# Performance work log

Measured on AMD Instinct MI355X. Metric: run time of the kernel, lower is better.

## Reference

```python
import jax, jax.numpy as jnp
import numpy as np

RADIUS = 9.0
GROUPS = 4
BLK = 64  # row block for streaming the N x N pairwise convolution


def leaky(x):
    return jnp.where(x >= 0, x, 0.2 * x)


def group_norm(x, gamma, beta, eps=1e-5):
    # x: (N, C); matches torch.nn.GroupNorm(GROUPS, C) applied to (1, C, N)
    N, C = x.shape
    xg = x.T.reshape(GROUPS, (C // GROUPS) * N)
    m = xg.mean(axis=1, keepdims=True)
    v = ((xg - m) ** 2).mean(axis=1, keepdims=True)
    xg = (xg - m) / jnp.sqrt(v + eps)
    return xg.reshape(C, N).T * gamma + beta


def tangent_vectors(n):
    # Duff et al. orthonormal tangent basis; n: (N,3) unit normals -> (N,2,3)
    x, y, z = n[:, 0], n[:, 1], n[:, 2]
    s = jnp.where(z >= 0, 1.0, -1.0)
    a = -1.0 / (s + z)
    b = x * y * a
    uv = jnp.stack([1 + s * x * x * a, s * b, -s * x, b, s + y * y * a, -y], axis=-1)
    return uv.reshape(-1, 2, 3)


def load_mesh(xyz, normals, weights):
    # Build oriented local frames nuv (N,3,3) as in dMaSIFConv_seg.load_mesh
    p = xyz / RADIUS
    uv = tangent_vectors(normals)                  # (N,2,3)
    diff = p[None, :, :] - p[:, None, :]           # (N,N,3): x_j - x_i
    d2 = jnp.sum(diff * diff, axis=-1)             # (N,N)
    cos = normals @ normals.T                      # (N,N)
    window = jnp.exp(-d2 * (2.0 - cos) ** 2)       # pseudo-geodesic Gaussian
    X = jnp.einsum('ikd,ijd->ijk', uv, diff)       # (N,N,2) tangent coords
    ov = jnp.einsum('ij,j,ijk->ik', window, weights[:, 0], X) + 1e-5  # (N,2)
    nrm = jnp.maximum(jnp.linalg.norm(ov, axis=-1, keepdims=True), 1e-12)
    ov = ov / nrm                                  # F.normalize
    ex, ey = ov[:, :1], ov[:, 1:]
    u, v = uv[:, 0, :], uv[:, 1, :]
    return jnp.stack([normals, ex * u + ey * v, -ey * u + ex * v], axis=1)


def dmasif_conv(points, nuv, feats,
                ni_w1, ni_b1, ni_w2, ni_b2, gn_in_g, gn_in_b,
                cv_a1, cv_b1, cv_a2, cv_b2,
                no_w1, no_b1, no_w2, no_b2, gn_out_g, gn_out_b):
    N = points.shape[0]
    H = ni_w1.shape[0]
    O = no_w1.shape[0]
    # net_in + GroupNorm
    h = leaky(feats @ ni_w1.T + ni_b1)
    h = leaky(h @ ni_w2.T + ni_b2)
    h = group_norm(h, gn_in_g, gn_in_b)            # (N,H)
    p = points / (np.sqrt(2.0) * RADIUS)
    n = jax.lax.stop_gradient(nuv[:, 0, :])        # normals detached in window

    p_blk = p.reshape(-1, BLK, 3)
    n_blk = n.reshape(-1, BLK, 3)
    nuv_blk = nuv.reshape(-1, BLK, 3, 3)

    @jax.checkpoint
    def step(carry, blk):
        pi, ni, nuvi = blk                                  # (B,3),(B,3),(B,3,3)
        diff = p[None, :, :] - pi[:, None, :]               # (B,N,3)
        d2 = jnp.sum(diff * diff, axis=-1)                  # (B,N)
        window = jnp.exp(-d2 * (2.0 - ni @ n.T) ** 2)       # (B,N)
        X = jnp.einsum('bkd,bnd->bnk', nuvi, diff)          # (B,N,3) local coords
        g = jax.nn.relu(jnp.einsum('bnk,ck->bnc', X, cv_a1) + cv_b1)  # (B,N,8)
        M = jax.nn.relu(jnp.einsum('bnc,fc->bnf', g, cv_a2) + cv_b2)  # (B,N,H*O)
        M = M.reshape(BLK, N, O, H)
        out = jnp.einsum('bn,bnoh,nh->bo', window, M, h)    # (B,O)
        return carry, out

    _, outs = jax.lax.scan(step, None, (p_blk, n_blk, nuv_blk))
    y = outs.reshape(N, O)
    y = leaky(y @ no_w1.T + no_b1)
    y = leaky(y @ no_w2.T + no_b2)
    return group_norm(y, gn_out_g, gn_out_b)


def setup_inputs() -> dict:
    key = jax.random.key(0)
    ks = jax.random.split(key, 32)
    N, I, U, H, O, C = 4096, 16, 16, 16, 16, 8
    nrm = jax.random.normal(ks[1], (N, 3), dtype=jnp.float32)
    nrm = nrm / jnp.linalg.norm(nrm, axis=-1, keepdims=True)
    w = lambda k, sh: 0.1 * jax.random.normal(k, sh, dtype=jnp.float32)
    return {
        'surface_xyz': 10.0 * jax.random.normal(ks[0], (N, 3), dtype=jnp.float32),
        'surface_normals': nrm,
        'features': jax.random.normal(ks[2], (N, I), dtype=jnp.float32),
        'os_w1': w(ks[3], (U, I)), 'os_b1': w(ks[4], (U,)),
        'os_w2': w(ks[5], (1, U)), 'os_b2': w(ks[6], (1,)),
        'ni_w1': w(ks[7], (H, I)), 'ni_b1': w(ks[8], (H,)),
        'ni_w2': w(ks[9], (H, H)), 'ni_b2': w(ks[10], (H,)),
        'gn_in_g': jnp.ones((H,), jnp.float32), 'gn_in_b': jnp.zeros((H,), jnp.float32),
        'cv_a1': w(ks[11], (C, 3)), 'cv_b1': w(ks[12], (C,)),
        'cv_a2': w(ks[13], (H * O, C)), 'cv_b2': w(ks[14], (H * O,)),
        'no_w1': w(ks[15], (O, H)), 'no_b1': w(ks[16], (O,)),
        'no_w2': w(ks[17], (O, O)), 'no_b2': w(ks[18], (O,)),
        'gn_out_g': jnp.ones((O,), jnp.float32), 'gn_out_b': jnp.zeros((O,), jnp.float32),
        'll_w1': w(ks[19], (O, O)), 'll_b1': w(ks[20], (O,)),
        'll_w2': w(ks[21], (O, O)), 'll_b2': w(ks[22], (O,)),
        'lt_w': w(ks[23], (O, I)), 'lt_b': w(ks[24], (O,)),
    }


def reference(surface_xyz, surface_normals, features,
              os_w1, os_b1, os_w2, os_b2,
              ni_w1, ni_b1, ni_w2, ni_b2, gn_in_g, gn_in_b,
              cv_a1, cv_b1, cv_a2, cv_b2,
              no_w1, no_b1, no_w2, no_b2, gn_out_g, gn_out_b,
              ll_w1, ll_b1, ll_w2, ll_b2, lt_w, lt_b):
    # orientation scores: Linear -> LeakyReLU(0.2) -> Linear
    scores = leaky(features @ os_w1.T + os_b1) @ os_w2.T + os_b2  # (N,1)
    nuv = load_mesh(surface_xyz, surface_normals, scores)
    # dMaSIFConv_seg forward, n_layers = 1
    x_i = dmasif_conv(surface_xyz, nuv, features,
                      ni_w1, ni_b1, ni_w2, ni_b2, gn_in_g, gn_in_b,
                      cv_a1, cv_b1, cv_a2, cv_b2,
                      no_w1, no_b1, no_w2, no_b2, gn_out_g, gn_out_b)
    x_i = jax.nn.relu(x_i @ ll_w1.T + ll_b1) @ ll_w2.T + ll_b2  # linear_layers[0]
    x = features @ lt_w.T + lt_b                                 # linear_transform[0]
    return x + x_i
```

## Files before the change

kernel.cpp:

```cpp
#include <hip/hip_runtime.h>

#define NP 4096
#define NJC 32
#define JCH (NP / NJC)
#define HR  12

typedef const float* fp;

using half4  = __attribute__((ext_vector_type(4))) __fp16;
using fp16x2 = __attribute__((ext_vector_type(2))) __fp16;
using f32x4  = __attribute__((ext_vector_type(4))) float;

__device__ __forceinline__ float lk(float x) { return x >= 0.f ? x : 0.2f * x; }

__device__ __forceinline__ unsigned int pkrtz(float a, float b) {
    fp16x2 h = __builtin_amdgcn_cvt_pkrtz(a, b);
    unsigned int u; __builtin_memcpy(&u, &h, 4); return u;
}
__device__ __forceinline__ fp16x2 u2h(unsigned int u) {
    fp16x2 h; __builtin_memcpy(&h, &u, 4); return h;
}
__device__ __forceinline__ fp16x2 pkmax0(fp16x2 a, fp16x2 z) {
    fp16x2 d;
    asm("v_pk_max_f16 %0, %1, %2" : "=v"(d) : "v"(a), "v"(z));
    return d;
}

#define OFF_ACC   0
#define OFF_OV    16
#define OFF_CONV  (16 + 2*NP)
#define ZERO_FLTS (16 + 2*NP + 16*NP)
#define OFF_SC    ZERO_FLTS
#define OFF_UV    (OFF_SC  + NP)
#define OFF_P9    (OFF_UV  + 6*NP)
#define OFF_NRM   (OFF_P9  + 3*NP)
#define OFF_HPRE  (OFF_NRM + 3*NP)
#define OFF_HNRM  (OFF_HPRE+ 16*NP)
#define OFF_NUV   (OFF_HNRM+ 16*NP)
#define OFF_Y2    (OFF_NUV + 9*NP)
#define WS_FLTS   (OFF_Y2  + 16*NP)

__global__ __launch_bounds__(256) void k_prep(
    fp xyz, fp nrm, fp feats,
    fp osw1, fp osb1, fp osw2, fp osb2,
    fp niw1, fp nib1, fp niw2, fp nib2,
    float* __restrict__ ws)
{
    const int i = blockIdx.x * 256 + threadIdx.x;

    float f[16];
#pragma unroll
    for (int c = 0; c < 16; c++) f[c] = feats[i * 16 + c];

    float sc = osb2[0];
#pragma unroll
    for (int u = 0; u < 16; u++) {
        float a = osb1[u];
#pragma unroll
        for (int c = 0; c < 16; c++) a += osw1[u * 16 + c] * f[c];
        sc += osw2[u] * lk(a);
    }
    ws[OFF_SC + i] = sc;

    float h1[16];
#pragma unroll
    for (int u = 0; u < 16; u++) {
        float a = nib1[u];
#pragma unroll
        for (int c = 0; c < 16; c++) a += niw1[u * 16 + c] * f[c];
        h1[u] = lk(a);
    }
    float h2[16];
#pragma unroll
    for (int u = 0; u < 16; u++) {
        float a = nib2[u];
#pragma unroll
        for (int c = 0; c < 16; c++) a += niw2[u * 16 + c] * h1[c];
        h2[u] = lk(a);
        ws[OFF_HPRE + i * 16 + u] = h2[u];
    }

#pragma unroll
    for (int g = 0; g < 4; g++) {
        float s = 0.f, ss = 0.f;
#pragma unroll
        for (int k = 0; k < 4; k++) { float v = h2[g * 4 + k]; s += v; ss += v * v; }
#pragma unroll
        for (int off = 32; off > 0; off >>= 1) {
            s  += __shfl_down(s,  off);
            ss += __shfl_down(ss, off);
        }
        if ((threadIdx.x & 63) == 0) {
            atomicAdd(&ws[OFF_ACC + g],     s);
            atomicAdd(&ws[OFF_ACC + 4 + g], ss);
        }
    }

    float nx = nrm[i * 3], ny = nrm[i * 3 + 1], nz = nrm[i * 3 + 2];
    float s  = (nz >= 0.f) ? 1.f : -1.f;
    float a  = -1.f / (s + nz);
    float b  = nx * ny * a;
    float ux = 1.f + s * nx * nx * a, uy = s * b,            uz = -s * nx;
    float vx = b,                     vy = s + ny * ny * a,  vz = -ny;
    ws[OFF_UV + i * 6 + 0] = ux; ws[OFF_UV + i * 6 + 1] = uy; ws[OFF_UV + i * 6 + 2] = uz;
    ws[OFF_UV + i * 6 + 3] = vx; ws[OFF_UV + i * 6 + 4] = vy; ws[OFF_UV + i * 6 + 5] = vz;
    const float IR = 1.f / 9.f;
    ws[OFF_P9 + i * 3 + 0] = xyz[i * 3 + 0] * IR;
    ws[OFF_P9 + i * 3 + 1] = xyz[i * 3 + 1] * IR;
    ws[OFF_P9 + i * 3 + 2] = xyz[i * 3 + 2] * IR;
    ws[OFF_NRM + i * 3 + 0] = nx;
    ws[OFF_NRM + i * 3 + 1] = ny;
    ws[OFF_NRM + i * 3 + 2] = nz;
}

__global__ __launch_bounds__(256) void k_mesh(float* __restrict__ ws)
{
    __shared__ float sp[3][512];
    __shared__ float sn[3][512];
    __shared__ float ssc[512];
    __shared__ float red[256][2];

    const int tid = threadIdx.x;
    const int ib = blockIdx.x >> 3, jc = blockIdx.x & 7;
    const int il = tid & 63, sub = tid >> 6;
    const int i = ib * 64 + il;
    const int j0 = jc * 512;

    for (int t = tid; t < 512; t += 256) {
        int j = j0 + t;
        sp[0][t] = ws[OFF_P9 + j * 3];     sp[1][t] = ws[OFF_P9 + j * 3 + 1];  sp[2][t] = ws[OFF_P9 + j * 3 + 2];
        sn[0][t] = ws[OFF_NRM + j * 3];    sn[1][t] = ws[OFF_NRM + j * 3 + 1]; sn[2][t] = ws[OFF_NRM + j * 3 + 2];
        ssc[t]   = ws[OFF_SC + j];
    }
    __syncthreads();

    const float pix = ws[OFF_P9 + i * 3], piy = ws[OFF_P9 + i * 3 + 1], piz = ws[OFF_P9 + i * 3 + 2];
    const float nix = ws[OFF_NRM + i * 3], niy = ws[OFF_NRM + i * 3 + 1], niz = ws[OFF_NRM + i * 3 + 2];
    const float ux = ws[OFF_UV + i * 6],     uy = ws[OFF_UV + i * 6 + 1], uz = ws[OFF_UV + i * 6 + 2];
    const float vx = ws[OFF_UV + i * 6 + 3], vy = ws[OFF_UV + i * 6 + 4], vz = ws[OFF_UV + i * 6 + 5];

    float ov0 = 0.f, ov1 = 0.f;
#pragma unroll 4
    for (int t = 0; t < 128; t++) {
        int j = sub * 128 + t;
        float dx = sp[0][j] - pix, dy = sp[1][j] - piy, dz = sp[2][j] - piz;
        float d2 = dx * dx + dy * dy + dz * dz;
        float cs = nix * sn[0][j] + niy * sn[1][j] + niz * sn[2][j];
        float tt = 2.f - cs;
        float w  = __expf(-d2 * tt * tt) * ssc[j];
        ov0 += w * (ux * dx + uy * dy + uz * dz);
        ov1 += w * (vx * dx + vy * dy + vz * dz);
    }
    red[tid][0] = ov0; red[tid][1] = ov1;
    __syncthreads();
    if (sub == 0) {
        float a = ov0 + red[64 + il][0] + red[128 + il][0] + red[192 + il][0];
        float b = ov1 + red[64 + il][1] + red[128 + il][1] + red[192 + il][1];
        atomicAdd(&ws[OFF_OV + i * 2],     a);
        atomicAdd(&ws[OFF_OV + i * 2 + 1], b);
    }
}

__global__ __launch_bounds__(256) void k_fin(float* __restrict__ ws, fp gng, fp gnb)
{
    const int i = blockIdx.x * 256 + threadIdx.x;

    float o0 = ws[OFF_OV + i * 2]     + 1e-5f;
    float o1 = ws[OFF_OV + i * 2 + 1] + 1e-5f;
    float nr = fmaxf(sqrtf(o0 * o0 + o1 * o1), 1e-12f);
    float ex = o0 / nr, ey = o1 / nr;

    const float ux = ws[OFF_UV + i * 6],     uy = ws[OFF_UV + i * 6 + 1], uz = ws[OFF_UV + i * 6 + 2];
    const float vx = ws[OFF_UV + i * 6 + 3], vy = ws[OFF_UV + i * 6 + 4], vz = ws[OFF_UV + i * 6 + 5];
    const float nx = ws[OFF_NRM + i * 3], ny = ws[OFF_NRM + i * 3 + 1], nz = ws[OFF_NRM + i * 3 + 2];

    ws[OFF_NUV + i * 9 + 0] = nx;
    ws[OFF_NUV + i * 9 + 1] = ny;
    ws[OFF_NUV + i * 9 + 2] = nz;
    ws[OFF_NUV + i * 9 + 3] =  ex * ux + ey * vx;
    ws[OFF_NUV + i * 9 + 4] =  ex * uy + ey * vy;
    ws[OFF_NUV + i * 9 + 5] =  ex * uz + ey * vz;
    ws[OFF_NUV + i * 9 + 6] = -ey * ux + ex * vx;
    ws[OFF_NUV + i * 9 + 7] = -ey * uy + ex * vy;
    ws[OFF_NUV + i * 9 + 8] = -ey * uz + ex * vz;

    const float invM = 1.f / (4.f * NP);
#pragma unroll
    for (int c = 0; c < 16; c++) {
        int g = c >> 2;
        float m   = ws[OFF_ACC + g] * invM;
        float var = ws[OFF_ACC + 4 + g] * invM - m * m;
        float inv = rsqrtf(var + 1e-5f);
        ws[OFF_HNRM + i * 16 + c] =
            (ws[OFF_HPRE + i * 16 + c] - m) * inv * gng[c] + gnb[c];
    }
}

__global__ __launch_bounds__(256, 4) void k_conv(
    const float* __restrict__ ws,
    const float* __restrict__ cva1, const float* __restrict__ cvb1,
    const float* __restrict__ A2,   const float* __restrict__ B2,
    float* __restrict__ conv)
{
    __shared__ float4 sP[JCH];
    __shared__ float4 sN[JCH];
    __shared__ __align__(16) unsigned int sH2[JCH * HR];

    const int tid  = threadIdx.x;
    const int ib   = blockIdx.x >> 5;
    const int jc   = blockIdx.x & 31;
    const int j0   = jc * JCH;
    const int lane = tid & 63;
    const int wv   = tid >> 6;
    const int o    = lane & 15;
    const int quad = lane >> 4;
    const float IVS2 = 0.70710678118654752f;

    if (tid < JCH) {
        const int t = tid;
        const int j = j0 + t;
        sP[t] = make_float4(ws[OFF_P9 + j * 3] * IVS2,
                            ws[OFF_P9 + j * 3 + 1] * IVS2,
                            ws[OFF_P9 + j * 3 + 2] * IVS2, 0.f);
        sN[t] = make_float4(ws[OFF_NRM + j * 3],
                            ws[OFF_NRM + j * 3 + 1],
                            ws[OFF_NRM + j * 3 + 2], 0.f);
        const float4* hs = (const float4*)(ws + OFF_HNRM + j * 16);
        float4 h0 = hs[0], h1 = hs[1], h2 = hs[2], h3 = hs[3];
        uint4 w0, w1;
        w0.x = pkrtz(h0.x, h0.y); w0.y = pkrtz(h0.z, h0.w);
        w0.z = pkrtz(h1.x, h1.y); w0.w = pkrtz(h1.z, h1.w);
        w1.x = pkrtz(h2.x, h2.y); w1.y = pkrtz(h2.z, h2.w);
        w1.z = pkrtz(h3.x, h3.y); w1.w = pkrtz(h3.z, h3.w);
        *(uint4*)(sH2 + t * HR)     = w0;
        *(uint4*)(sH2 + t * HR + 4) = w1;
    }

    half4 Bf[16];
#pragma unroll
    for (int t = 0; t < 16; t++) {
        half4 v = {(__fp16)0.f, (__fp16)0.f, (__fp16)0.f, (__fp16)0.f};
        const float* row = A2 + (o * 16 + t) * 8;
        if (quad == 0) {
#pragma unroll
            for (int c = 0; c < 4; c++) v[c] = (__fp16)row[c];
        } else if (quad == 1) {
#pragma unroll
            for (int c = 0; c < 4; c++) v[c] = (__fp16)row[4 + c];
        } else if (quad == 2) {
            v[0] = (__fp16)B2[o * 16 + t];
        }
        Bf[t] = v;
    }

    float a1[24], b1c[8];
#pragma unroll
    for (int k = 0; k < 24; k++) a1[k] = cva1[k];
#pragma unroll
    for (int k = 0; k < 8; k++)  b1c[k] = cvb1[k];

    __syncthreads();

    const f32x4 zc = {0.f, 0.f, 0.f, 0.f};
    const fp16x2 h2z = {(__fp16)0.f, (__fp16)0.f};
    const int o4 = o << 2;

#pragma unroll 1
    for (int ii = 0; ii < 16; ii++) {
        const int i = ib * 64 + wv * 16 + ii;
        const float pix = ws[OFF_P9 + i * 3 + 0] * IVS2;
        const float piy = ws[OFF_P9 + i * 3 + 1] * IVS2;
        const float piz = ws[OFF_P9 + i * 3 + 2] * IVS2;
        float r[9];
#pragma unroll
        for (int k = 0; k < 9; k++) r[k] = ws[OFF_NUV + i * 9 + k];

        float acc[8];
#pragma unroll
        for (int k = 0; k < 8; k++) acc[k] = 0.f;

#pragma unroll 1
        for (int jg = 0; jg < JCH / 64; jg++) {
            const int jl = jg * 64 + lane;
            const float4 pj = sP[jl];
            const float4 nj = sN[jl];
            const float dx = pj.x - pix, dy = pj.y - piy, dz = pj.z - piz;
            const float d2 = dx * dx + dy * dy + dz * dz;
            const float cs = r[0] * nj.x + r[1] * nj.y + r[2] * nj.z;
            const float tt = 2.f - cs;
            const float wwin = __expf(-d2 * tt * tt);
            const float X0 = r[0] * dx + r[1] * dy + r[2] * dz;
            const float X1 = r[3] * dx + r[4] * dy + r[5] * dz;
            const float X2 = r[6] * dx + r[7] * dy + r[8] * dz;
            float g[8];
#pragma unroll
            for (int c = 0; c < 8; c++)
                g[c] = fmaxf(a1[c * 3] * X0 + a1[c * 3 + 1] * X1 +
                             a1[c * 3 + 2] * X2 + b1c[c], 0.f);
            const int wg0 = (int)pkrtz(wwin * g[0], wwin * g[1]);
            const int wg1 = (int)pkrtz(wwin * g[2], wwin * g[3]);
            const int wg2 = (int)pkrtz(wwin * g[4], wwin * g[5]);
            const int wg3 = (int)pkrtz(wwin * g[6], wwin * g[7]);
            const int whp = (int)pkrtz(wwin, 0.f);

#pragma unroll 2
            for (int tau = 0; tau < 4; tau++) {
                const int srcb = tau * 64 + o4;
                const unsigned u0 = (unsigned)__builtin_amdgcn_ds_bpermute(srcb, wg0);
                const unsigned u1 = (unsigned)__builtin_amdgcn_ds_bpermute(srcb, wg1);
                const unsigned u2 = (unsigned)__builtin_amdgcn_ds_bpermute(srcb, wg2);
                const unsigned u3 = (unsigned)__builtin_amdgcn_ds_bpermute(srcb, wg3);
                const unsigned uw = (unsigned)__builtin_amdgcn_ds_bpermute(srcb, whp);

                const uint4* hb = (const uint4*)(sH2 + (jg * 64 + tau * 16 + quad * 4) * HR);
                uint4 ha[8];
                ha[0] = hb[0]; ha[1] = hb[1];
                ha[2] = hb[3]; ha[3] = hb[4];
                ha[4] = hb[6]; ha[5] = hb[7];
                ha[6] = hb[9]; ha[7] = hb[10];

                uint2 av;
                av.x = (quad == 0) ? u0 : (quad == 1) ? u2 : (quad == 2) ? uw : 0u;
                av.y = (quad == 0) ? u1 : (quad == 1) ? u3 : 0u;
                half4 Af; __builtin_memcpy(&Af, &av, 8);

#pragma unroll
                for (int hq = 0; hq < 2; hq++) {
                    fp16x2 P[16];
#pragma unroll
                    for (int q2 = 0; q2 < 4; q2++) {
                        const int q = hq * 4 + q2;
                        f32x4 C0 = __builtin_amdgcn_mfma_f32_16x16x16f16(Af, Bf[2 * q],     zc, 0, 0, 0);
                        f32x4 C1 = __builtin_amdgcn_mfma_f32_16x16x16f16(Af, Bf[2 * q + 1], zc, 0, 0, 0);
#pragma unroll
                        for (int r2 = 0; r2 < 4; r2++) {
                            fp16x2 pp = __builtin_amdgcn_cvt_pkrtz(C0[r2], C1[r2]);
                            P[r2 * 4 + q2] = pkmax0(pp, h2z);
                        }
                    }
#pragma unroll
                    for (int r2 = 0; r2 < 4; r2++) {
                        const uint4 h4 = ha[r2 * 2 + hq];
                        float a = acc[hq * 4 + r2];
                        a = __builtin_amdgcn_fdot2(P[r2 * 4 + 0], u2h(h4.x), a, false);
                        a = __builtin_amdgcn_fdot2(P[r2 * 4 + 1], u2h(h4.y), a, false);
                        a = __builtin_amdgcn_fdot2(P[r2 * 4 + 2], u2h(h4.z), a, false);
                        a = __builtin_amdgcn_fdot2(P[r2 * 4 + 3], u2h(h4.w), a, false);
                        acc[hq * 4 + r2] = a;
                    }
                }
            }
        }

        float accO = ((acc[0] + acc[1]) + (acc[2] + acc[3]))
                   + ((acc[4] + acc[5]) + (acc[6] + acc[7]));
        accO += __shfl_xor(accO, 16, 64);
        accO += __shfl_xor(accO, 32, 64);
        if (lane < 16) atomicAdd(&conv[i * 16 + o], accO);
    }
}

__global__ __launch_bounds__(256) void k_post1(
    float* __restrict__ ws, fp now1, fp nob1, fp now2, fp nob2)
{
    const int i = blockIdx.x * 256 + threadIdx.x;
    float cv[16];
#pragma unroll
    for (int o = 0; o < 16; o++) cv[o] = ws[OFF_CONV + i * 16 + o];

    float y1[16];
#pragma unroll
    for (int u = 0; u < 16; u++) {
        float a = nob1[u];
#pragma unroll
        for (int k = 0; k < 16; k++) a += now1[u * 16 + k] * cv[k];
        y1[u] = lk(a);
    }
    float y2[16];
#pragma unroll
    for (int u = 0; u < 16; u++) {
        float a = nob2[u];
#pragma unroll
        for (int k = 0; k < 16; k++) a += now2[u * 16 + k] * y1[k];
        y2[u] = lk(a);
        ws[OFF_Y2 + i * 16 + u] = y2[u];
    }
#pragma unroll
    for (int g = 0; g < 4; g++) {
        float s = 0.f, ss = 0.f;
#pragma unroll
        for (int k = 0; k < 4; k++) { float v = y2[g * 4 + k]; s += v; ss += v * v; }
#pragma unroll
        for (int off = 32; off > 0; off >>= 1) {
            s  += __shfl_down(s,  off);
            ss += __shfl_down(ss, off);
        }
        if ((threadIdx.x & 63) == 0) {
            atomicAdd(&ws[OFF_ACC + 8 + g],  s);
            atomicAdd(&ws[OFF_ACC + 12 + g], ss);
        }
    }
}

__global__ __launch_bounds__(256) void k_post2(
    const float* __restrict__ ws, fp feats, fp gg, fp gb,
    fp llw1, fp llb1, fp llw2, fp llb2, fp ltw, fp ltb,
    float* __restrict__ out)
{
    const int i = blockIdx.x * 256 + threadIdx.x;
    const float invM = 1.f / (4.f * NP);

    float z[16];
#pragma unroll
    for (int c = 0; c < 16; c++) {
        int g = c >> 2;
        float m   = ws[OFF_ACC + 8 + g] * invM;
        float var = ws[OFF_ACC + 12 + g] * invM - m * m;
        float inv = rsqrtf(var + 1e-5f);
        z[c] = (ws[OFF_Y2 + i * 16 + c] - m) * inv * gg[c] + gb[c];
    }
    float r1[16];
#pragma unroll
    for (int o = 0; o < 16; o++) {
        float a = llb1[o];
#pragma unroll
        for (int k = 0; k < 16; k++) a += llw1[o * 16 + k] * z[k];
        r1[o] = fmaxf(a, 0.f);
    }
    float f[16];
#pragma unroll
    for (int c = 0; c < 16; c++) f[c] = feats[i * 16 + c];
#pragma unroll
    for (int o = 0; o < 16; o++) {
        float a = llb2[o];
#pragma unroll
        for (int k = 0; k < 16; k++) a += llw2[o * 16 + k] * r1[k];
        float x = ltb[o];
#pragma unroll
        for (int k = 0; k < 16; k++) x += ltw[o * 16 + k] * f[k];
        out[i * 16 + o] = x + a;
    }
}

extern "C" void kernel_launch(void* const* d_in, const int* in_sizes, int n_in,
                              void* d_out, int out_size, void* d_ws, size_t ws_size,
                              hipStream_t stream)
{
    fp xyz  = (fp)d_in[0];
    fp nrm  = (fp)d_in[1];
    fp fts  = (fp)d_in[2];
    fp osw1 = (fp)d_in[3],  osb1 = (fp)d_in[4],  osw2 = (fp)d_in[5],  osb2 = (fp)d_in[6];
    fp niw1 = (fp)d_in[7],  nib1 = (fp)d_in[8],  niw2 = (fp)d_in[9],  nib2 = (fp)d_in[10];
    fp gng  = (fp)d_in[11], gnb  = (fp)d_in[12];
    fp cva1 = (fp)d_in[13], cvb1 = (fp)d_in[14], cva2 = (fp)d_in[15], cvb2 = (fp)d_in[16];
    fp now1 = (fp)d_in[17], nob1 = (fp)d_in[18], now2 = (fp)d_in[19], nob2 = (fp)d_in[20];
    fp gog  = (fp)d_in[21], gob  = (fp)d_in[22];
    fp llw1 = (fp)d_in[23], llb1 = (fp)d_in[24], llw2 = (fp)d_in[25], llb2 = (fp)d_in[26];
    fp ltw  = (fp)d_in[27], ltb  = (fp)d_in[28];

    float* ws = (float*)d_ws;

    (void)hipMemsetAsync(d_ws, 0, (size_t)ZERO_FLTS * sizeof(float), stream);
    k_prep<<<NP / 256, 256, 0, stream>>>(xyz, nrm, fts,
                                         osw1, osb1, osw2, osb2,
                                         niw1, nib1, niw2, nib2, ws);
    k_mesh<<<512, 256, 0, stream>>>(ws);
    k_fin<<<NP / 256, 256, 0, stream>>>(ws, gng, gnb);
    k_conv<<<64 * NJC, 256, 0, stream>>>(ws, cva1, cvb1, cva2, cvb2, ws + OFF_CONV);
    k_post1<<<NP / 256, 256, 0, stream>>>(ws, now1, nob1, now2, nob2);
    k_post2<<<NP / 256, 256, 0, stream>>>(ws, fts, gog, gob,
                                          llw1, llb1, llw2, llb2, ltw, ltb,
                                          (float*)d_out);
}
```

Baseline: 510.5 us.

## Process four query points per j-chunk pass to reuse LDS loads

Restructures the conv loop so each wave handles four i points at once inside the j loop. Each shared-memory load of pj/nj and the H tile can then be reused across four i instead of being reloaded per i. The next point's bpermutes are issued before the current point's MFMA work so their latency can overlap with compute. In exchange, register pressure rises (wg[4][5], eight accumulators, and per-i r/p values reloaded from global memory inside the j loop), and the tau loop is no longer unrolled.

```diff
diff --git a/kernel.cpp b/kernel.cpp
--- a/kernel.cpp
+++ b/kernel.cpp
@@ -266,51 +266,58 @@
     const int o4 = o << 2;
 
 #pragma unroll 1
-    for (int ii = 0; ii < 16; ii++) {
-        const int i = ib * 64 + wv * 16 + ii;
-        const float pix = ws[OFF_P9 + i * 3 + 0] * IVS2;
-        const float piy = ws[OFF_P9 + i * 3 + 1] * IVS2;
-        const float piz = ws[OFF_P9 + i * 3 + 2] * IVS2;
-        float r[9];
-#pragma unroll
-        for (int k = 0; k < 9; k++) r[k] = ws[OFF_NUV + i * 9 + k];
-
-        float acc[8];
-#pragma unroll
-        for (int k = 0; k < 8; k++) acc[k] = 0.f;
+    for (int it = 0; it < 4; it++) {
+        const int ibase = ib * 64 + wv * 16 + it * 4;
+        float accA[4], accB[4];
+#pragma unroll
+        for (int k = 0; k < 4; k++) { accA[k] = 0.f; accB[k] = 0.f; }
 
 #pragma unroll 1
         for (int jg = 0; jg < JCH / 64; jg++) {
             const int jl = jg * 64 + lane;
             const float4 pj = sP[jl];
             const float4 nj = sN[jl];
-            const float dx = pj.x - pix, dy = pj.y - piy, dz = pj.z - piz;
-            const float d2 = dx * dx + dy * dy + dz * dz;
-            const float cs = r[0] * nj.x + r[1] * nj.y + r[2] * nj.z;
-            const float tt = 2.f - cs;
-            const float wwin = __expf(-d2 * tt * tt);
-            const float X0 = r[0] * dx + r[1] * dy + r[2] * dz;
-            const float X1 = r[3] * dx + r[4] * dy + r[5] * dz;
-            const float X2 = r[6] * dx + r[7] * dy + r[8] * dz;
-            float g[8];
-#pragma unroll
-            for (int c = 0; c < 8; c++)
-                g[c] = fmaxf(a1[c * 3] * X0 + a1[c * 3 + 1] * X1 +
-                             a1[c * 3 + 2] * X2 + b1c[c], 0.f);
-            const int wg0 = (int)pkrtz(wwin * g[0], wwin * g[1]);
-            const int wg1 = (int)pkrtz(wwin * g[2], wwin * g[3]);
-            const int wg2 = (int)pkrtz(wwin * g[4], wwin * g[5]);
-            const int wg3 = (int)pkrtz(wwin * g[6], wwin * g[7]);
-            const int whp = (int)pkrtz(wwin, 0.f);
-
-#pragma unroll 2
+
+            unsigned wg[4][5];
+#pragma unroll
+            for (int ii = 0; ii < 4; ii++) {
+                const int i = ibase + ii;
+                const float pix = ws[OFF_P9 + i * 3 + 0] * IVS2;
+                const float piy = ws[OFF_P9 + i * 3 + 1] * IVS2;
+                const float piz = ws[OFF_P9 + i * 3 + 2] * IVS2;
+                float r[9];
+#pragma unroll
+                for (int k = 0; k < 9; k++) r[k] = ws[OFF_NUV + i * 9 + k];
+
+                const float dx = pj.x - pix, dy = pj.y - piy, dz = pj.z - piz;
+                const float d2 = dx * dx + dy * dy + dz * dz;
+                const float cs = r[0] * nj.x + r[1] * nj.y + r[2] * nj.z;
+                const float tt = 2.f - cs;
+                const float wwin = __expf(-d2 * tt * tt);
+                const float X0 = r[0] * dx + r[1] * dy + r[2] * dz;
+                const float X1 = r[3] * dx + r[4] * dy + r[5] * dz;
+                const float X2 = r[6] * dx + r[7] * dy + r[8] * dz;
+                float g[8];
+#pragma unroll
+                for (int c = 0; c < 8; c++)
+                    g[c] = fmaxf(a1[c * 3] * X0 + a1[c * 3 + 1] * X1 +
+                                 a1[c * 3 + 2] * X2 + b1c[c], 0.f);
+                wg[ii][0] = pkrtz(wwin * g[0], wwin * g[1]);
+                wg[ii][1] = pkrtz(wwin * g[2], wwin * g[3]);
+                wg[ii][2] = pkrtz(wwin * g[4], wwin * g[5]);
+                wg[ii][3] = pkrtz(wwin * g[6], wwin * g[7]);
+                wg[ii][4] = pkrtz(wwin, 0.f);
+            }
+
+#pragma unroll 1
             for (int tau = 0; tau < 4; tau++) {
                 const int srcb = tau * 64 + o4;
-                const unsigned u0 = (unsigned)__builtin_amdgcn_ds_bpermute(srcb, wg0);
-                const unsigned u1 = (unsigned)__builtin_amdgcn_ds_bpermute(srcb, wg1);
-                const unsigned u2 = (unsigned)__builtin_amdgcn_ds_bpermute(srcb, wg2);
-                const unsigned u3 = (unsigned)__builtin_amdgcn_ds_bpermute(srcb, wg3);
-                const unsigned uw = (unsigned)__builtin_amdgcn_ds_bpermute(srcb, whp);
+
+                unsigned u0 = (unsigned)__builtin_amdgcn_ds_bpermute(srcb, (int)wg[0][0]);
+                unsigned u1 = (unsigned)__builtin_amdgcn_ds_bpermute(srcb, (int)wg[0][1]);
+                unsigned u2 = (unsigned)__builtin_amdgcn_ds_bpermute(srcb, (int)wg[0][2]);
+                unsigned u3 = (unsigned)__builtin_amdgcn_ds_bpermute(srcb, (int)wg[0][3]);
+                unsigned u4 = (unsigned)__builtin_amdgcn_ds_bpermute(srcb, (int)wg[0][4]);
 
                 const uint4* hb = (const uint4*)(sH2 + (jg * 64 + tau * 16 + quad * 4) * HR);
                 uint4 ha[8];
@@ -319,44 +326,58 @@
                 ha[4] = hb[6]; ha[5] = hb[7];
                 ha[6] = hb[9]; ha[7] = hb[10];
 
-                uint2 av;
-                av.x = (quad == 0) ? u0 : (quad == 1) ? u2 : (quad == 2) ? uw : 0u;
-                av.y = (quad == 0) ? u1 : (quad == 1) ? u3 : 0u;
-                half4 Af; __builtin_memcpy(&Af, &av, 8);
-
-#pragma unroll
-                for (int hq = 0; hq < 2; hq++) {
-                    fp16x2 P[16];
-#pragma unroll
-                    for (int q2 = 0; q2 < 4; q2++) {
-                        const int q = hq * 4 + q2;
-                        f32x4 C0 = __builtin_amdgcn_mfma_f32_16x16x16f16(Af, Bf[2 * q],     zc, 0, 0, 0);
-                        f32x4 C1 = __builtin_amdgcn_mfma_f32_16x16x16f16(Af, Bf[2 * q + 1], zc, 0, 0, 0);
+#pragma unroll
+                for (int ii = 0; ii < 4; ii++) {
+                    uint2 av;
+                    av.x = (quad == 0) ? u0 : (quad == 1) ? u2 : (quad == 2) ? u4 : 0u;
+                    av.y = (quad == 0) ? u1 : (quad == 1) ? u3 : 0u;
+                    if (ii < 3) {
+                        u0 = (unsigned)__builtin_amdgcn_ds_bpermute(srcb, (int)wg[ii + 1][0]);
+                        u1 = (unsigned)__builtin_amdgcn_ds_bpermute(srcb, (int)wg[ii + 1][1]);
+                        u2 = (unsigned)__builtin_amdgcn_ds_bpermute(srcb, (int)wg[ii + 1][2]);
+                        u3 = (unsigned)__builtin_amdgcn_ds_bpermute(srcb, (int)wg[ii + 1][3]);
+                        u4 = (unsigned)__builtin_amdgcn_ds_bpermute(srcb, (int)wg[ii + 1][4]);
+                    }
+                    half4 Af; __builtin_memcpy(&Af, &av, 8);
+
+                    float aA = accA[ii], aB = accB[ii];
+#pragma unroll
+                    for (int hq = 0; hq < 2; hq++) {
+                        fp16x2 P[16];
+#pragma unroll
+                        for (int q2 = 0; q2 < 4; q2++) {
+                            const int q = hq * 4 + q2;
+                            f32x4 C0 = __builtin_amdgcn_mfma_f32_16x16x16f16(Af, Bf[2 * q],     zc, 0, 0, 0);
+                            f32x4 C1 = __builtin_amdgcn_mfma_f32_16x16x16f16(Af, Bf[2 * q + 1], zc, 0, 0, 0);
+#pragma unroll
+                            for (int r2 = 0; r2 < 4; r2++) {
+                                fp16x2 pp = __builtin_amdgcn_cvt_pkrtz(C0[r2], C1[r2]);
+                                P[r2 * 4 + q2] = pkmax0(pp, h2z);
+                            }
+                        }
+                        float a = (hq == 0) ? aA : aB;
 #pragma unroll
                         for (int r2 = 0; r2 < 4; r2++) {
-                            fp16x2 pp = __builtin_amdgcn_cvt_pkrtz(C0[r2], C1[r2]);
-                            P[r2 * 4 + q2] = pkmax0(pp, h2z);
+                            const uint4 h4 = ha[r2 * 2 + hq];
+                            a = __builtin_amdgcn_fdot2(P[r2 * 4 + 0], u2h(h4.x), a, false);
+                            a = __builtin_amdgcn_fdot2(P[r2 * 4 + 1], u2h(h4.y), a, false);
+                            a = __builtin_amdgcn_fdot2(P[r2 * 4 + 2], u2h(h4.z), a, false);
+                            a = __builtin_amdgcn_fdot2(P[r2 * 4 + 3], u2h(h4.w), a, false);
                         }
+                        if (hq == 0) aA = a; else aB = a;
                     }
-#pragma unroll
-                    for (int r2 = 0; r2 < 4; r2++) {
-                        const uint4 h4 = ha[r2 * 2 + hq];
-                        float a = acc[hq * 4 + r2];
-                        a = __builtin_amdgcn_fdot2(P[r2 * 4 + 0], u2h(h4.x), a, false);
-                        a = __builtin_amdgcn_fdot2(P[r2 * 4 + 1], u2h(h4.y), a, false);
-                        a = __builtin_amdgcn_fdot2(P[r2 * 4 + 2], u2h(h4.z), a, false);
-                        a = __builtin_amdgcn_fdot2(P[r2 * 4 + 3], u2h(h4.w), a, false);
-                        acc[hq * 4 + r2] = a;
-                    }
+                    accA[ii] = aA; accB[ii] = aB;
                 }
             }
         }
 
-        float accO = ((acc[0] + acc[1]) + (acc[2] + acc[3]))
-                   + ((acc[4] + acc[5]) + (acc[6] + acc[7]));
-        accO += __shfl_xor(accO, 16, 64);
-        accO += __shfl_xor(accO, 32, 64);
-        if (lane < 16) atomicAdd(&conv[i * 16 + o], accO);
+#pragma unroll
+        for (int ii = 0; ii < 4; ii++) {
+            float accO = accA[ii] + accB[ii];
+            accO += __shfl_xor(accO, 16, 64);
+            accO += __shfl_xor(accO, 32, 64);
+            if (lane < 16) atomicAdd(&conv[(ibase + ii) * 16 + o], accO);
+        }
     }
 }
 
```

New measurement: 541.4 us. 6.1% more time.
